# Performance work log

Measured on AMD Instinct MI355X. Metric: run time of the kernel, lower is better.

## Reference

```python
import jax, jax.numpy as jnp
import numpy as np

B = 64
RX, RZ, RX_, RZ_ = 32, 16, 16, 8
TN = 1
STRIDE = 2
IN_DIM, OUT_DIM = 256, 512
KEY_DIM, H, ATTN_RATIO = 32, 8, 2
D = ATTN_RATIO * KEY_DIM            # per-head value dim = 64
DH = D * H                          # 512
NH_KD = KEY_DIM * H                 # 256
N = RX * RX + TN * RZ * RZ          # 1280 tokens (search + template)
N_ = RX_ * RX_ + TN * RZ_ * RZ_     # 320 subsampled query tokens
SCALE = KEY_DIM ** -0.5
EPS = 1e-5


def linear_bn(x, W, gamma, beta):
    # Linear (no bias) followed by BatchNorm1d in training mode over (B*N, C)
    y = jnp.einsum('bnc,oc->bno', x, W)
    m = y.mean(axis=(0, 1))
    v = y.var(axis=(0, 1))  # biased variance, as torch BN uses for normalization
    return (y - m) * jax.lax.rsqrt(v + EPS) * gamma + beta


def subsample(x):
    # stride-subsample the search-region tokens and each template's tokens
    b, n, c = x.shape
    parts = [x[:, :RX * RX].reshape(b, RX, RX, c)[:, ::STRIDE, ::STRIDE].reshape(b, -1, c)]
    for i in range(TN):
        s = RX * RX + i * RZ * RZ
        z = x[:, s:s + RZ * RZ].reshape(b, RZ, RZ, c)[:, ::STRIDE, ::STRIDE].reshape(b, -1, c)
        parts.append(z)
    return jnp.concatenate(parts, axis=1)


def setup_inputs() -> dict:
    key = jax.random.key(0)
    ks = jax.random.split(key, 4)
    return {
        'x': jax.random.normal(ks[0], (B, N, IN_DIM), dtype=jnp.float32),
        'W_kv': jax.random.normal(ks[1], (NH_KD + DH, IN_DIM), dtype=jnp.float32) * 0.02,
        'g_kv': jnp.ones((NH_KD + DH,), jnp.float32),
        'b_kv': jnp.zeros((NH_KD + DH,), jnp.float32),
        'W_q': jax.random.normal(ks[2], (NH_KD, IN_DIM), dtype=jnp.float32) * 0.02,
        'g_q': jnp.ones((NH_KD,), jnp.float32),
        'b_q': jnp.zeros((NH_KD,), jnp.float32),
        'W_p': jax.random.normal(ks[3], (OUT_DIM, DH), dtype=jnp.float32) * 0.02,
        'g_p': jnp.ones((OUT_DIM,), jnp.float32),
        'b_p': jnp.zeros((OUT_DIM,), jnp.float32),
    }


def reference(x, W_kv, g_kv, b_kv, W_q, g_q, b_q, W_p, g_p, b_p):
    b = x.shape[0]
    # fused KV projection + BN, then split into per-head K and V
    kv = linear_bn(x, W_kv, g_kv, b_kv).reshape(b, N, H, KEY_DIM + D)
    k = kv[..., :KEY_DIM].transpose(0, 2, 1, 3)   # [B,H,N,key_dim]
    v = kv[..., KEY_DIM:].transpose(0, 2, 1, 3)   # [B,H,N,d]
    # Q: subsample tokens, then Linear_BN
    q = linear_bn(subsample(x), W_q, g_q, b_q).reshape(b, N_, H, KEY_DIM).transpose(0, 2, 1, 3)
    attn = jax.nn.softmax(jnp.einsum('bhqd,bhkd->bhqk', q, k) * SCALE, axis=-1)
    o = jnp.einsum('bhqk,bhkd->bhqd', attn, v).transpose(0, 2, 1, 3).reshape(b, N_, DH)
    return linear_bn(jax.nn.hard_swish(o), W_p, g_p, b_p)
```

## Files before the change

kernel.cpp:

```cpp
#include <hip/hip_runtime.h>
#include <hip/hip_bf16.h>
#include <math.h>

#define EPSF 1e-5f
#define SCALEF 0.17677669529663687f

typedef unsigned short u16;
typedef unsigned int u32;
typedef __attribute__((ext_vector_type(8))) short bf16x8;
typedef __attribute__((ext_vector_type(4))) float f32x4;

__device__ __forceinline__ float b2f(u16 u) {
    union { unsigned int i; float f; } v; v.i = ((unsigned int)u) << 16; return v.f;
}
__device__ __forceinline__ u16 f2b(float f) {
    union { float f; unsigned int i; } v; v.f = f;
    unsigned int x = v.i;
    return (u16)((x + 0x7fffu + ((x >> 16) & 1u)) >> 16);
}

__global__ void convert_f32_bf16(const float* __restrict__ src, u16* __restrict__ dst, int n4) {
    int i = blockIdx.x * 256 + threadIdx.x;
    if (i >= n4) return;
    float4 v = ((const float4*)src)[i];
    ushort4 o;
    o.x = f2b(v.x); o.y = f2b(v.y); o.z = f2b(v.z); o.w = f2b(v.w);
    ((ushort4*)dst)[i] = o;
}

__global__ void gather_sub_bf16(const u16* __restrict__ xb, u16* __restrict__ xsub, int n8) {
    int i = blockIdx.x * 256 + threadIdx.x;
    if (i >= n8) return;
    int e = i << 3;
    int row = e >> 8;
    int col = e & 255;
    int b = row / 320;
    int t = row - b * 320;
    int n;
    if (t < 256) n = ((t >> 4) << 6) + ((t & 15) << 1);
    else { int tt = t - 256; n = 1024 + ((tt >> 3) << 5) + ((tt & 7) << 1); }
    *(int4*)(xsub + e) = *(const int4*)(xb + ((size_t)(b * 1280 + n)) * 256 + col);
}

template<int OUT_F32>
__global__ __launch_bounds__(256) void gemm_bt(const u16* __restrict__ A, const u16* __restrict__ Bw,
                                               void* __restrict__ Cv, int M, int N, int K,
                                               float* __restrict__ sums) {
    __shared__ u16 As[128 * 40];
    __shared__ u16 Bs[128 * 40];
    __shared__ float sumbuf[4][64][2];
    const int tid = threadIdx.x;
    const int wave = tid >> 6, lane = tid & 63;
    const int quad = lane >> 4, lc = lane & 15;
    const int wr = wave >> 1, wc = wave & 1;
    const int m0 = blockIdx.x * 128, n0 = blockIdx.y * 128;
    const int lrow = tid >> 2;
    const int lk = (tid & 3) << 3;

    f32x4 acc[4][4];
#pragma unroll
    for (int i = 0; i < 4; ++i)
#pragma unroll
        for (int j = 0; j < 4; ++j) acc[i][j] = (f32x4){0.f, 0.f, 0.f, 0.f};

    for (int k0 = 0; k0 < K; k0 += 32) {
        __syncthreads();
        *(int4*)&As[lrow * 40 + lk]        = *(const int4*)(A  + (size_t)(m0 + lrow) * K + k0 + lk);
        *(int4*)&As[(lrow + 64) * 40 + lk] = *(const int4*)(A  + (size_t)(m0 + lrow + 64) * K + k0 + lk);
        *(int4*)&Bs[lrow * 40 + lk]        = *(const int4*)(Bw + (size_t)(n0 + lrow) * K + k0 + lk);
        *(int4*)&Bs[(lrow + 64) * 40 + lk] = *(const int4*)(Bw + (size_t)(n0 + lrow + 64) * K + k0 + lk);
        __syncthreads();
        bf16x8 af[4], bfr[4];
#pragma unroll
        for (int mi = 0; mi < 4; ++mi) af[mi]  = *(const bf16x8*)&As[(wr * 64 + mi * 16 + lc) * 40 + quad * 8];
#pragma unroll
        for (int ni = 0; ni < 4; ++ni) bfr[ni] = *(const bf16x8*)&Bs[(wc * 64 + ni * 16 + lc) * 40 + quad * 8];
#pragma unroll
        for (int mi = 0; mi < 4; ++mi)
#pragma unroll
            for (int ni = 0; ni < 4; ++ni)
                acc[mi][ni] = __builtin_amdgcn_mfma_f32_16x16x32_bf16(af[mi], bfr[ni], acc[mi][ni], 0, 0, 0);
    }
    float ps[4], ps2[4];
#pragma unroll
    for (int ni = 0; ni < 4; ++ni) { ps[ni] = 0.f; ps2[ni] = 0.f; }
#pragma unroll
    for (int mi = 0; mi < 4; ++mi)
#pragma unroll
        for (int ni = 0; ni < 4; ++ni)
#pragma unroll
            for (int r = 0; r < 4; ++r) {
                int row = m0 + wr * 64 + mi * 16 + quad * 4 + r;
                int cn  = n0 + wc * 64 + ni * 16 + lc;
                float v = acc[mi][ni][r];
                ps[ni] += v; ps2[ni] += v * v;
                if (OUT_F32) ((float*)Cv)[(size_t)row * N + cn] = v;
                else         ((u16*)Cv)[(size_t)row * N + cn] = f2b(v);
            }
#pragma unroll
    for (int ni = 0; ni < 4; ++ni) {
        ps[ni]  += __shfl_xor(ps[ni], 16);  ps[ni]  += __shfl_xor(ps[ni], 32);
        ps2[ni] += __shfl_xor(ps2[ni], 16); ps2[ni] += __shfl_xor(ps2[ni], 32);
    }
    if (quad == 0) {
#pragma unroll
        for (int ni = 0; ni < 4; ++ni) {
            sumbuf[wave][ni * 16 + lc][0] = ps[ni];
            sumbuf[wave][ni * 16 + lc][1] = ps2[ni];
        }
    }
    __syncthreads();
    {
        int which = tid & 1, idx = (tid >> 1) & 63, wcg = tid >> 7;
        int channel = n0 + wcg * 64 + idx;
        float v = sumbuf[wcg][idx][which] + sumbuf[wcg + 2][idx][which];
        int rep = blockIdx.x & 7;
        atomicAdd(&sums[(rep * 2 + which) * N + channel], v);
    }
}

__global__ void finalize_bn(const float* __restrict__ sum2, const float* __restrict__ g,
                            const float* __restrict__ beta, int cols, float inv_n, float scale,
                            float* __restrict__ AB) {
    int c = blockIdx.x * 256 + threadIdx.x;
    if (c >= cols) return;
    float s = 0.f, s2 = 0.f;
#pragma unroll
    for (int r = 0; r < 8; ++r) {
        s  += sum2[(r * 2 + 0) * cols + c];
        s2 += sum2[(r * 2 + 1) * cols + c];
    }
    float m = s * inv_n;
    float var = s2 * inv_n - m * m;
    float a = g[c] * rsqrtf(var + EPSF) * scale;
    AB[c] = a;
    AB[cols + c] = beta[c] * scale - m * a;
}

__global__ __launch_bounds__(256) void normalize_kv(const u16* __restrict__ kv, const float* __restrict__ AB,
                                                    u16* __restrict__ Kn, u16* __restrict__ Vtn) {
    __shared__ u16 Vs[64 * 66];
    const int h = blockIdx.x, nt = blockIdx.y, b = blockIdx.z;
    const int bh = b * 8 + h;
    const int tid = threadIdx.x;
    {
        int tok = tid >> 2, dk = (tid & 3) << 3;
        size_t src = ((size_t)(b * 1280 + nt * 64 + tok)) * 768 + h * 96 + dk;
        union { int4 v; u16 u[8]; } ld; ld.v = *(const int4*)(kv + src);
        union { int4 v; u16 u[8]; } st;
#pragma unroll
        for (int j = 0; j < 8; ++j) {
            int c = h * 96 + dk + j;
            st.u[j] = f2b(b2f(ld.u[j]) * AB[c] + AB[768 + c]);
        }
        int g = tok >> 5, kk = tok & 31;
        int rowp = nt * 64 + g * 32 + ((kk & 1) << 4) + (kk >> 1);
        *(int4*)(Kn + ((size_t)bh * 1280 + rowp) * 32 + dk) = st.v;
    }
#pragma unroll
    for (int half = 0; half < 2; ++half) {
        int t = (tid >> 3) + half * 32;
        int dv = (tid & 7) << 3;
        size_t src = ((size_t)(b * 1280 + nt * 64 + t)) * 768 + h * 96 + 32 + dv;
        union { int4 v; u16 u[8]; } ld; ld.v = *(const int4*)(kv + src);
#pragma unroll
        for (int j = 0; j < 8; ++j) {
            int c = h * 96 + 32 + dv + j;
            Vs[(dv + j) * 66 + t] = f2b(b2f(ld.u[j]) * AB[c] + AB[768 + c]);
        }
    }
    __syncthreads();
#pragma unroll
    for (int half = 0; half < 2; ++half) {
        int d = (tid >> 3) + half * 32;
        int tc = (tid & 7) << 3;
        union { int4 v; u16 u[8]; } st;
#pragma unroll
        for (int j = 0; j < 8; ++j) st.u[j] = Vs[d * 66 + tc + j];
        *(int4*)(Vtn + ((size_t)bh * 64 + d) * 1280 + nt * 64 + tc) = st.v;
    }
}

__global__ __launch_bounds__(256, 2) void attn_kernel3(const u16* __restrict__ Kn, const u16* __restrict__ Vtn,
                                                       const u16* __restrict__ q_raw, const float* __restrict__ ABq,
                                                       u16* __restrict__ o_act) {
    __shared__ u16 Ps[4 * 5 * 640];
    const int tid = threadIdx.x;
    const int wave = tid >> 6, lane = tid & 63;
    const int quad = lane >> 4, lc = lane & 15;
    const int h = blockIdx.x, b = blockIdx.y;
    const int bh = b * 8 + h;

    float qa[8], qb[8];
#pragma unroll
    for (int j = 0; j < 8; ++j) { int c = h * 32 + quad * 8 + j; qa[j] = ABq[c]; qb[j] = ABq[256 + c]; }
    bf16x8 qf[5];
#pragma unroll
    for (int j = 0; j < 5; ++j) {
        const u16* qs = q_raw + ((size_t)(b * 320 + j * 64 + wave * 16 + lc)) * 256 + h * 32 + quad * 8;
        union { int4 v; u16 u[8]; } ld; ld.v = *(const int4*)qs;
        union { bf16x8 v; u16 u[8]; } st;
#pragma unroll
        for (int jj = 0; jj < 8; ++jj) st.u[jj] = f2b(b2f(ld.u[jj]) * qa[jj] + qb[jj]);
        qf[j] = st.v;
    }

    const u16* Kp = Kn + (size_t)bh * 1280 * 32 + lc * 32 + quad * 8;
    const u16* Vp = Vtn + (size_t)bh * 64 * 1280 + lc * 1280 + quad * 8;
    u16* Pw = &Ps[wave * 5 * 640];

    f32x4 acc[5][4];
#pragma unroll
    for (int j = 0; j < 5; ++j)
#pragma unroll
        for (int i = 0; i < 4; ++i) acc[j][i] = (f32x4){0.f, 0.f, 0.f, 0.f};
    float lsum[5][4];
#pragma unroll
    for (int j = 0; j < 5; ++j)
#pragma unroll
        for (int r = 0; r < 4; ++r) lsum[j][r] = 0.f;

    for (int kc = 0; kc < 1280; kc += 32) {
        bf16x8 kf0 = *(const bf16x8*)(Kp + kc * 32);
        bf16x8 kf1 = *(const bf16x8*)(Kp + kc * 32 + 512);
        bf16x8 vf0 = *(const bf16x8*)(Vp + kc);
        bf16x8 vf1 = *(const bf16x8*)(Vp + 16 * 1280 + kc);
        bf16x8 vf2 = *(const bf16x8*)(Vp + 32 * 1280 + kc);
        bf16x8 vf3 = *(const bf16x8*)(Vp + 48 * 1280 + kc);
        f32x4 z = (f32x4){0.f, 0.f, 0.f, 0.f};
        f32x4 s0[5], s1[5];
#pragma unroll
        for (int j = 0; j < 5; ++j) {
            s0[j] = __builtin_amdgcn_mfma_f32_16x16x32_bf16(qf[j], kf0, z, 0, 0, 0);
            s1[j] = __builtin_amdgcn_mfma_f32_16x16x32_bf16(qf[j], kf1, z, 0, 0, 0);
        }
#pragma unroll
        for (int j = 0; j < 5; ++j)
#pragma unroll
            for (int r = 0; r < 4; ++r) {
                float p0 = __expf(s0[j][r]);
                float p1 = __expf(s1[j][r]);
                lsum[j][r] += p0 + p1;
                u32 pk = (u32)f2b(p0) | ((u32)f2b(p1) << 16);
                *(u32*)&Pw[j * 640 + (quad * 4 + r) * 40 + 2 * lc] = pk;
            }
#pragma unroll
        for (int j = 0; j < 5; ++j) {
            bf16x8 pf = *(const bf16x8*)&Pw[j * 640 + lc * 40 + quad * 8];
            acc[j][0] = __builtin_amdgcn_mfma_f32_16x16x32_bf16(pf, vf0, acc[j][0], 0, 0, 0);
            acc[j][1] = __builtin_amdgcn_mfma_f32_16x16x32_bf16(pf, vf1, acc[j][1], 0, 0, 0);
            acc[j][2] = __builtin_amdgcn_mfma_f32_16x16x32_bf16(pf, vf2, acc[j][2], 0, 0, 0);
            acc[j][3] = __builtin_amdgcn_mfma_f32_16x16x32_bf16(pf, vf3, acc[j][3], 0, 0, 0);
        }
    }
#pragma unroll
    for (int j = 0; j < 5; ++j) {
        float inv[4];
#pragma unroll
        for (int r = 0; r < 4; ++r) {
            float l = lsum[j][r];
            l += __shfl_xor(l, 1);
            l += __shfl_xor(l, 2);
            l += __shfl_xor(l, 4);
            l += __shfl_xor(l, 8);
            inv[r] = 1.f / l;
        }
        int qrow = b * 320 + j * 64 + wave * 16 + quad * 4;
#pragma unroll
        for (int nt = 0; nt < 4; ++nt)
#pragma unroll
            for (int r = 0; r < 4; ++r) {
                float o = acc[j][nt][r] * inv[r];
                float hs = o * fminf(fmaxf(o + 3.f, 0.f), 6.f) * (1.f / 6.f);
                o_act[(size_t)(qrow + r) * 512 + h * 64 + nt * 16 + lc] = f2b(hs);
            }
    }
}

__global__ void bn_apply_out(const float* __restrict__ praw, const float* __restrict__ ABp,
                             float* __restrict__ out, int n4) {
    int i = blockIdx.x * 256 + threadIdx.x;
    if (i >= n4) return;
    int e = i << 2;
    int c = e & 511;
    float4 v = ((const float4*)praw)[i];
    float4 o;
    o.x = v.x * ABp[c]     + ABp[512 + c];
    o.y = v.y * ABp[c + 1] + ABp[512 + c + 1];
    o.z = v.z * ABp[c + 2] + ABp[512 + c + 2];
    o.w = v.w * ABp[c + 3] + ABp[512 + c + 3];
    ((float4*)out)[i] = o;
}

extern "C" void kernel_launch(void* const* d_in, const int* in_sizes, int n_in,
                              void* d_out, int out_size, void* d_ws, size_t ws_size,
                              hipStream_t stream) {
    const float* x   = (const float*)d_in[0];
    const float* Wkv = (const float*)d_in[1];
    const float* gkv = (const float*)d_in[2];
    const float* bkv = (const float*)d_in[3];
    const float* Wq  = (const float*)d_in[4];
    const float* gq  = (const float*)d_in[5];
    const float* bq  = (const float*)d_in[6];
    const float* Wp  = (const float*)d_in[7];
    const float* gp  = (const float*)d_in[8];
    const float* bp  = (const float*)d_in[9];
    float* out = (float*)d_out;

    char* ws = (char*)d_ws;
    size_t off = 0;
    auto alloc = [&](size_t bytes) -> void* {
        void* p = ws + off;
        off += (bytes + 255) & ~(size_t)255;
        return p;
    };
    u16*   kv_raw = (u16*)alloc(81920ull * 768 * 2);
    u16*   q_raw  = (u16*)alloc(20480ull * 256 * 2);
    void*  slot1  = alloc(81920ull * 256 * 2);
    u16*   x_b    = (u16*)slot1;
    u16*   K_norm = (u16*)slot1;
    float* p_raw  = (float*)slot1;
    void*  slot2  = alloc(20480ull * 512 * 2);
    u16*   xsub_b = (u16*)slot2;
    u16*   o_act  = (u16*)slot2;
    u16*   Vt_norm = (u16*)alloc(512ull * 64 * 1280 * 2);
    u16*   Wkv_b  = (u16*)alloc(768ull * 256 * 2);
    u16*   Wq_b   = (u16*)alloc(256ull * 256 * 2);
    u16*   Wp_b   = (u16*)alloc(512ull * 512 * 2);
    float* sums_kv = (float*)alloc(8 * 2 * 768 * sizeof(float));
    float* sums_q  = (float*)alloc(8 * 2 * 256 * sizeof(float));
    float* sums_p  = (float*)alloc(8 * 2 * 512 * sizeof(float));
    float* ABkv = (float*)alloc(1536 * sizeof(float));
    float* ABq  = (float*)alloc(512 * sizeof(float));
    float* ABp  = (float*)alloc(1024 * sizeof(float));

    dim3 blk(256);
    hipMemsetAsync(sums_kv, 0, 8 * 2 * (768 + 256 + 512) * sizeof(float), stream);

    convert_f32_bf16<<<20480, blk, 0, stream>>>(x,   x_b,   5242880);
    convert_f32_bf16<<<192,   blk, 0, stream>>>(Wkv, Wkv_b, 49152);
    convert_f32_bf16<<<64,    blk, 0, stream>>>(Wq,  Wq_b,  16384);
    convert_f32_bf16<<<256,   blk, 0, stream>>>(Wp,  Wp_b,  65536);
    gather_sub_bf16<<<2560,   blk, 0, stream>>>(x_b, xsub_b, 655360);

    gemm_bt<0><<<dim3(640, 6), blk, 0, stream>>>(x_b, Wkv_b, kv_raw, 81920, 768, 256, sums_kv);
    gemm_bt<0><<<dim3(160, 2), blk, 0, stream>>>(xsub_b, Wq_b, q_raw, 20480, 256, 256, sums_q);

    finalize_bn<<<3, blk, 0, stream>>>(sums_kv, gkv, bkv, 768, 1.f / 81920.f, 1.f, ABkv);
    finalize_bn<<<1, blk, 0, stream>>>(sums_q,  gq,  bq,  256, 1.f / 20480.f, SCALEF, ABq);

    normalize_kv<<<dim3(8, 20, 64), blk, 0, stream>>>(kv_raw, ABkv, K_norm, Vt_norm);

    attn_kernel3<<<dim3(8, 64), blk, 0, stream>>>(K_norm, Vt_norm, q_raw, ABq, o_act);

    gemm_bt<1><<<dim3(160, 4), blk, 0, stream>>>(o_act, Wp_b, p_raw, 20480, 512, 512, sums_p);
    finalize_bn<<<2, blk, 0, stream>>>(sums_p, gp, bp, 512, 1.f / 20480.f, 1.f, ABp);

    bn_apply_out<<<10240, blk, 0, stream>>>(p_raw, ABp, out, 2621440);
}
```

Before: 423.2 us.

## Keep softmax probabilities in registers by transposing QK MFMA and permuting K rows

The attention kernel now computes S^T (K as the A operand, Q as B), so each lane's exp outputs already sit in the layout the PV MFMA needs as its B operand. This removes the per-chunk shared-memory round trip for P. K rows are re-permuted in normalize_kv to match the new fragment order. The exp is replaced by a native exp2 with log2(e) folded into the Q scale, and bf16 packing uses the hardware v_cvt_pk_bf16_f32 instruction. The row-sum reduction and output stores change to match the transposed layout, and the stores are now vectorised 4-wide. Correctness depends on the K-row permutation matching the MFMA operand layout exactly.

```diff
diff --git a/kernel.cpp b/kernel.cpp
--- a/kernel.cpp
+++ b/kernel.cpp
@@ -4,6 +4,7 @@
 
 #define EPSF 1e-5f
 #define SCALEF 0.17677669529663687f
+#define LOG2E 1.4426950408889634f
 
 typedef unsigned short u16;
 typedef unsigned int u32;
@@ -17,6 +18,18 @@
     union { float f; unsigned int i; } v; v.f = f;
     unsigned int x = v.i;
     return (u16)((x + 0x7fffu + ((x >> 16) & 1u)) >> 16);
+}
+__device__ __forceinline__ float fexp2(float x) {
+#if __has_builtin(__builtin_amdgcn_exp2f)
+    return __builtin_amdgcn_exp2f(x);
+#else
+    return exp2f(x);
+#endif
+}
+__device__ __forceinline__ u32 cvtpk_bf16(float lo, float hi) {
+    u32 r;
+    asm("v_cvt_pk_bf16_f32 %0, %1, %2" : "=v"(r) : "v"(lo), "v"(hi));
+    return r;
 }
 
 __global__ void convert_f32_bf16(const float* __restrict__ src, u16* __restrict__ dst, int n4) {
@@ -154,7 +167,7 @@
             st.u[j] = f2b(b2f(ld.u[j]) * AB[c] + AB[768 + c]);
         }
         int g = tok >> 5, kk = tok & 31;
-        int rowp = nt * 64 + g * 32 + ((kk & 1) << 4) + (kk >> 1);
+        int rowp = nt * 64 + g * 32 + ((kk & 4) << 2) + ((kk >> 3) << 2) + (kk & 3);
         *(int4*)(Kn + ((size_t)bh * 1280 + rowp) * 32 + dk) = st.v;
     }
 #pragma unroll
@@ -181,10 +194,9 @@
     }
 }
 
-__global__ __launch_bounds__(256, 2) void attn_kernel3(const u16* __restrict__ Kn, const u16* __restrict__ Vtn,
+__global__ __launch_bounds__(256, 2) void attn_kernel4(const u16* __restrict__ Kn, const u16* __restrict__ Vtn,
                                                        const u16* __restrict__ q_raw, const float* __restrict__ ABq,
                                                        u16* __restrict__ o_act) {
-    __shared__ u16 Ps[4 * 5 * 640];
     const int tid = threadIdx.x;
     const int wave = tid >> 6, lane = tid & 63;
     const int quad = lane >> 4, lc = lane & 15;
@@ -207,73 +219,71 @@
 
     const u16* Kp = Kn + (size_t)bh * 1280 * 32 + lc * 32 + quad * 8;
     const u16* Vp = Vtn + (size_t)bh * 64 * 1280 + lc * 1280 + quad * 8;
-    u16* Pw = &Ps[wave * 5 * 640];
 
     f32x4 acc[5][4];
 #pragma unroll
     for (int j = 0; j < 5; ++j)
 #pragma unroll
         for (int i = 0; i < 4; ++i) acc[j][i] = (f32x4){0.f, 0.f, 0.f, 0.f};
-    float lsum[5][4];
-#pragma unroll
-    for (int j = 0; j < 5; ++j)
-#pragma unroll
-        for (int r = 0; r < 4; ++r) lsum[j][r] = 0.f;
-
+    float lsum[5];
+#pragma unroll
+    for (int j = 0; j < 5; ++j) lsum[j] = 0.f;
+
+    const f32x4 z = (f32x4){0.f, 0.f, 0.f, 0.f};
     for (int kc = 0; kc < 1280; kc += 32) {
-        bf16x8 kf0 = *(const bf16x8*)(Kp + kc * 32);
-        bf16x8 kf1 = *(const bf16x8*)(Kp + kc * 32 + 512);
+        bf16x8 kfA = *(const bf16x8*)(Kp + kc * 32);
+        bf16x8 kfB = *(const bf16x8*)(Kp + kc * 32 + 512);
         bf16x8 vf0 = *(const bf16x8*)(Vp + kc);
         bf16x8 vf1 = *(const bf16x8*)(Vp + 16 * 1280 + kc);
         bf16x8 vf2 = *(const bf16x8*)(Vp + 32 * 1280 + kc);
         bf16x8 vf3 = *(const bf16x8*)(Vp + 48 * 1280 + kc);
-        f32x4 z = (f32x4){0.f, 0.f, 0.f, 0.f};
         f32x4 s0[5], s1[5];
 #pragma unroll
         for (int j = 0; j < 5; ++j) {
-            s0[j] = __builtin_amdgcn_mfma_f32_16x16x32_bf16(qf[j], kf0, z, 0, 0, 0);
-            s1[j] = __builtin_amdgcn_mfma_f32_16x16x32_bf16(qf[j], kf1, z, 0, 0, 0);
-        }
-#pragma unroll
-        for (int j = 0; j < 5; ++j)
+            s0[j] = __builtin_amdgcn_mfma_f32_16x16x32_bf16(kfA, qf[j], z, 0, 0, 0);
+            s1[j] = __builtin_amdgcn_mfma_f32_16x16x32_bf16(kfB, qf[j], z, 0, 0, 0);
+        }
+#pragma unroll
+        for (int j = 0; j < 5; ++j) {
+            float p0 = fexp2(s0[j][0]);
+            float p1 = fexp2(s0[j][1]);
+            float p2 = fexp2(s0[j][2]);
+            float p3 = fexp2(s0[j][3]);
+            float p4 = fexp2(s1[j][0]);
+            float p5 = fexp2(s1[j][1]);
+            float p6 = fexp2(s1[j][2]);
+            float p7 = fexp2(s1[j][3]);
+            lsum[j] += ((p0 + p1) + (p2 + p3)) + ((p4 + p5) + (p6 + p7));
+            union { u32 w[4]; bf16x8 v; } pf;
+            pf.w[0] = cvtpk_bf16(p0, p1);
+            pf.w[1] = cvtpk_bf16(p2, p3);
+            pf.w[2] = cvtpk_bf16(p4, p5);
+            pf.w[3] = cvtpk_bf16(p6, p7);
+            acc[j][0] = __builtin_amdgcn_mfma_f32_16x16x32_bf16(vf0, pf.v, acc[j][0], 0, 0, 0);
+            acc[j][1] = __builtin_amdgcn_mfma_f32_16x16x32_bf16(vf1, pf.v, acc[j][1], 0, 0, 0);
+            acc[j][2] = __builtin_amdgcn_mfma_f32_16x16x32_bf16(vf2, pf.v, acc[j][2], 0, 0, 0);
+            acc[j][3] = __builtin_amdgcn_mfma_f32_16x16x32_bf16(vf3, pf.v, acc[j][3], 0, 0, 0);
+        }
+    }
+#pragma unroll
+    for (int j = 0; j < 5; ++j) {
+        float l = lsum[j];
+        l += __shfl_xor(l, 16);
+        l += __shfl_xor(l, 32);
+        float inv = 1.f / l;
+        int qrow = b * 320 + j * 64 + wave * 16 + lc;
+        u16* dst = o_act + (size_t)qrow * 512 + h * 64 + quad * 4;
+#pragma unroll
+        for (int nt = 0; nt < 4; ++nt) {
+            ushort4 st;
 #pragma unroll
             for (int r = 0; r < 4; ++r) {
-                float p0 = __expf(s0[j][r]);
-                float p1 = __expf(s1[j][r]);
-                lsum[j][r] += p0 + p1;
-                u32 pk = (u32)f2b(p0) | ((u32)f2b(p1) << 16);
-                *(u32*)&Pw[j * 640 + (quad * 4 + r) * 40 + 2 * lc] = pk;
+                float o = acc[j][nt][r] * inv;
+                float hs = o * fminf(fmaxf(o + 3.f, 0.f), 6.f) * (1.f / 6.f);
+                ((u16*)&st)[r] = f2b(hs);
             }
-#pragma unroll
-        for (int j = 0; j < 5; ++j) {
-            bf16x8 pf = *(const bf16x8*)&Pw[j * 640 + lc * 40 + quad * 8];
-            acc[j][0] = __builtin_amdgcn_mfma_f32_16x16x32_bf16(pf, vf0, acc[j][0], 0, 0, 0);
-            acc[j][1] = __builtin_amdgcn_mfma_f32_16x16x32_bf16(pf, vf1, acc[j][1], 0, 0, 0);
-            acc[j][2] = __builtin_amdgcn_mfma_f32_16x16x32_bf16(pf, vf2, acc[j][2], 0, 0, 0);
-            acc[j][3] = __builtin_amdgcn_mfma_f32_16x16x32_bf16(pf, vf3, acc[j][3], 0, 0, 0);
-        }
-    }
-#pragma unroll
-    for (int j = 0; j < 5; ++j) {
-        float inv[4];
-#pragma unroll
-        for (int r = 0; r < 4; ++r) {
-            float l = lsum[j][r];
-            l += __shfl_xor(l, 1);
-            l += __shfl_xor(l, 2);
-            l += __shfl_xor(l, 4);
-            l += __shfl_xor(l, 8);
-            inv[r] = 1.f / l;
-        }
-        int qrow = b * 320 + j * 64 + wave * 16 + quad * 4;
-#pragma unroll
-        for (int nt = 0; nt < 4; ++nt)
-#pragma unroll
-            for (int r = 0; r < 4; ++r) {
-                float o = acc[j][nt][r] * inv[r];
-                float hs = o * fminf(fmaxf(o + 3.f, 0.f), 6.f) * (1.f / 6.f);
-                o_act[(size_t)(qrow + r) * 512 + h * 64 + nt * 16 + lc] = f2b(hs);
-            }
+            *(ushort4*)(dst + nt * 16) = st;
+        }
     }
 }
 
@@ -347,11 +357,11 @@
     gemm_bt<0><<<dim3(160, 2), blk, 0, stream>>>(xsub_b, Wq_b, q_raw, 20480, 256, 256, sums_q);
 
     finalize_bn<<<3, blk, 0, stream>>>(sums_kv, gkv, bkv, 768, 1.f / 81920.f, 1.f, ABkv);
-    finalize_bn<<<1, blk, 0, stream>>>(sums_q,  gq,  bq,  256, 1.f / 20480.f, SCALEF, ABq);
+    finalize_bn<<<1, blk, 0, stream>>>(sums_q,  gq,  bq,  256, 1.f / 20480.f, SCALEF * LOG2E, ABq);
 
     normalize_kv<<<dim3(8, 20, 64), blk, 0, stream>>>(kv_raw, ABkv, K_norm, Vt_norm);
 
-    attn_kernel3<<<dim3(8, 64), blk, 0, stream>>>(K_norm, Vt_norm, q_raw, ABq, o_act);
+    attn_kernel4<<<dim3(8, 64), blk, 0, stream>>>(K_norm, Vt_norm, q_raw, ABq, o_act);
 
     gemm_bt<1><<<dim3(160, 4), blk, 0, stream>>>(o_act, Wp_b, p_raw, 20480, 512, 512, sums_p);
     finalize_bn<<<2, blk, 0, stream>>>(sums_p, gp, bp, 512, 1.f / 20480.f, 1.f, ABp);
```

Result: faster. 398.7 us (-5.8%).
